# Kernel optimization log

Hardware: AMD Instinct MI355X
Metric: run time of the kernel (lower is better)

## Reference

```python
import jax, jax.numpy as jnp
import numpy as np

N = 256        # num_nodes
F = 256        # feature_dim
B = 32         # batch
DEG = 32       # out-degree per node -> E = N*DEG edges


def setup_inputs() -> dict:
    key = jax.random.key(0)
    k1, k2, k3, k4 = jax.random.split(key, 4)
    node_features = jax.random.normal(k1, (B, N, F), dtype=jnp.float32)
    # xavier_uniform for [N, N, F] tensor: fan_in = N*F, fan_out = N*F per torch default flattening
    limit = float(np.sqrt(6.0 / (N * F + N * F)))
    W = jax.random.uniform(k2, (N, N, F), dtype=jnp.float32, minval=-limit, maxval=limit)
    phase = jax.random.uniform(k3, (N, N), dtype=jnp.float32, minval=0.0, maxval=2.0 * np.pi)
    # topology: each node i has DEG outgoing connections (paths[i])
    src = jnp.repeat(jnp.arange(N, dtype=jnp.int64), DEG)              # [E]
    dst = jax.random.randint(k4, (N * DEG,), 0, N, dtype=jnp.int64)    # [E]
    return {"node_features": node_features, "W": W, "phase": phase, "src": src, "dst": dst}


def reference(node_features, W, phase, src, dst):
    # real(exp(i*phase)) == cos(phase); per-edge effective weight [E, F]
    eff_w = W[src, dst, :] * jnp.cos(phase[src, dst])[:, None]
    # gather source node features and scale: [B, E, F]
    signal = node_features[:, src, :] * eff_w[None, :, :]
    # scatter-add into destination nodes
    propagated = jnp.zeros_like(node_features).at[:, dst, :].add(signal)
    # normalization by out-degree of each node index (matches original indexing)
    n = node_features.shape[1]
    counts = jnp.zeros((n,), dtype=node_features.dtype).at[src].add(1.0)
    norm = jnp.maximum(counts, 1.0)
    return propagated / norm[None, :, None]
```

## Files before the change

kernel.cpp:

```cpp
#include <hip/hip_runtime.h>
#include <math.h>

#define NN 256
#define FF 256
#define BB 32
#define EE 8192
#define F4  (FF / 4)
#define NF4 (NN * F4)


#define CAP 64

__global__ __launch_bounds__(1024, 8) void fused_propagate_kernel(
    const float4* __restrict__ nf4,
    const float4* __restrict__ W4,
    const float*  __restrict__ phase,
    const int*    __restrict__ dst,
    float4*       __restrict__ out4)
{
    const int bid = blockIdx.x;
    const int d   = bid >> 1;
    const int h   = bid & 1;

    const int t    = threadIdx.x;
    const int lane = t & 63;
    const int wv   = t >> 6;

    __shared__ int          scnt[NN];
    __shared__ unsigned int s_pk[CAP / 4];
    __shared__ float        a_list[CAP];
    __shared__ int          wtot[4];
    __shared__ float4       aw4[CAP * 64];

    const int4* dstq = (const int4*)dst;
    const int4 v0 = dstq[t];
    const int4 v1 = dstq[t + 1024];
    int c0 = (v0.x == d) + (v0.y == d) + (v0.z == d) + (v0.w == d);
    int c1 = (v1.x == d) + (v1.y == d) + (v1.z == d) + (v1.w == d);
    #pragma unroll
    for (int off = 1; off < 8; off <<= 1) {
        c0 += __shfl_xor(c0, off, 64);
        c1 += __shfl_xor(c1, off, 64);
    }
    if ((t & 7) == 0) {
        scnt[t >> 3]         = c0;
        scnt[128 + (t >> 3)] = c1;
    }
    __syncthreads();

    int cnt = 0, ind = 0;
    if (t < NN) { cnt = scnt[t]; ind = (cnt > 0) ? 1 : 0; }

    const unsigned long long mask  = __ballot(ind);
    const int                below = __popcll(mask & ((1ULL << lane) - 1ULL));
    if (wv < 4 && lane == 0) wtot[wv] = __popcll(mask);
    __syncthreads();

    const int total = wtot[0] + wtot[1] + wtot[2] + wtot[3];
    int wbase = 0;
    #pragma unroll
    for (int w = 0; w < 4; w++) wbase += (w < wv) ? wtot[w] : 0;

    unsigned char* s8w = (unsigned char*)s_pk;
    if (ind) {
        const float a = (float)cnt * cosf(phase[t * NN + d]) * 0.03125f;
        const int pos = wbase + below;
        s8w[pos]    = (unsigned char)t;
        a_list[pos] = a;
    }
    const int n4 = (total + 3) & ~3;
    if (t < n4 - total) {
        s8w[total + t]    = 0;
        a_list[total + t] = 0.0f;
    }
    __syncthreads();

    const int drow = d * F4;
    const unsigned char* s8 = (const unsigned char*)s_pk;
    for (int slot = t; slot < (n4 << 6); slot += 1024) {
        const int   e = slot >> 6, f = slot & 63;
        const float a = a_list[e];
        float4 w = W4[(int)s8[e] * NF4 + drow + f];
        w.x *= a; w.y *= a; w.z *= a; w.w *= a;
        aw4[slot] = w;
    }
    __syncthreads();

    const int q = t & 63;
    const int b = h * 16 + (t >> 6);
    const float4* nfb = nf4 + b * NF4 + q;

    float4 acc = {0.f, 0.f, 0.f, 0.f};

    if (n4 > 0) {
        const unsigned int su = s_pk[0];
        float4 x0 = nfb[((su      ) & 255u) * 64];
        float4 x1 = nfb[((su >>  8) & 255u) * 64];
        float4 x2 = nfb[((su >> 16) & 255u) * 64];
        float4 x3 = nfb[((su >> 24)       ) * 64];

        for (int k = 4; k < n4; k += 4) {
            const unsigned int sn = s_pk[k >> 2];
            const float4 y0 = nfb[((sn      ) & 255u) * 64];
            const float4 y1 = nfb[((sn >>  8) & 255u) * 64];
            const float4 y2 = nfb[((sn >> 16) & 255u) * 64];
            const float4 y3 = nfb[((sn >> 24)       ) * 64];

            {
                const float4 a0 = aw4[(k - 4) * 64 + q];
                const float4 a1 = aw4[(k - 3) * 64 + q];
                const float4 a2 = aw4[(k - 2) * 64 + q];
                const float4 a3 = aw4[(k - 1) * 64 + q];
                acc.x = fmaf(x0.x, a0.x, acc.x); acc.y = fmaf(x0.y, a0.y, acc.y);
                acc.z = fmaf(x0.z, a0.z, acc.z); acc.w = fmaf(x0.w, a0.w, acc.w);
                acc.x = fmaf(x1.x, a1.x, acc.x); acc.y = fmaf(x1.y, a1.y, acc.y);
                acc.z = fmaf(x1.z, a1.z, acc.z); acc.w = fmaf(x1.w, a1.w, acc.w);
                acc.x = fmaf(x2.x, a2.x, acc.x); acc.y = fmaf(x2.y, a2.y, acc.y);
                acc.z = fmaf(x2.z, a2.z, acc.z); acc.w = fmaf(x2.w, a2.w, acc.w);
                acc.x = fmaf(x3.x, a3.x, acc.x); acc.y = fmaf(x3.y, a3.y, acc.y);
                acc.z = fmaf(x3.z, a3.z, acc.z); acc.w = fmaf(x3.w, a3.w, acc.w);
            }
            x0 = y0; x1 = y1; x2 = y2; x3 = y3;
        }

        {
            const float4 a0 = aw4[(n4 - 4) * 64 + q];
            const float4 a1 = aw4[(n4 - 3) * 64 + q];
            const float4 a2 = aw4[(n4 - 2) * 64 + q];
            const float4 a3 = aw4[(n4 - 1) * 64 + q];
            acc.x = fmaf(x0.x, a0.x, acc.x); acc.y = fmaf(x0.y, a0.y, acc.y);
            acc.z = fmaf(x0.z, a0.z, acc.z); acc.w = fmaf(x0.w, a0.w, acc.w);
            acc.x = fmaf(x1.x, a1.x, acc.x); acc.y = fmaf(x1.y, a1.y, acc.y);
            acc.z = fmaf(x1.z, a1.z, acc.z); acc.w = fmaf(x1.w, a1.w, acc.w);
            acc.x = fmaf(x2.x, a2.x, acc.x); acc.y = fmaf(x2.y, a2.y, acc.y);
            acc.z = fmaf(x2.z, a2.z, acc.z); acc.w = fmaf(x2.w, a2.w, acc.w);
            acc.x = fmaf(x3.x, a3.x, acc.x); acc.y = fmaf(x3.y, a3.y, acc.y);
            acc.z = fmaf(x3.z, a3.z, acc.z); acc.w = fmaf(x3.w, a3.w, acc.w);
        }
    }

    out4[b * NF4 + drow + q] = acc;
}

extern "C" void kernel_launch(void* const* d_in, const int* in_sizes, int n_in,
                              void* d_out, int out_size, void* d_ws, size_t ws_size,
                              hipStream_t stream) {
    const float* nf    = (const float*)d_in[0];
    const float* W     = (const float*)d_in[1];
    const float* phase = (const float*)d_in[2];
    const int*   dst   = (const int*)d_in[4];
    float*       out   = (float*)d_out;

    fused_propagate_kernel<<<512, 1024, 0, stream>>>(
        (const float4*)nf, (const float4*)W, phase, dst, (float4*)out);
}
```

Before: 117.9 us.

## Process all 32 batches per block and prefetch first features before weight staging

Each block now handles one destination node for all 32 batches (two accumulators per thread) instead of splitting batches across two blocks, halving the grid to 256 blocks. This avoids duplicating the dst histogram, phase/cos work and the W gather/scale into shared memory across two blocks. The first group of node-feature loads is also issued before the weight staging loop so their latency overlaps it. The cost is fewer blocks (256 for the whole GPU), more registers per thread and a lower launch-bounds occupancy hint.

New measurement: 114.6 us. -2.7%, faster.

```diff
diff --git a/kernel.cpp b/kernel.cpp
--- a/kernel.cpp
+++ b/kernel.cpp
@@ -11,17 +11,14 @@
 
 #define CAP 64
 
-__global__ __launch_bounds__(1024, 8) void fused_propagate_kernel(
+__global__ __launch_bounds__(1024, 4) void fused_propagate_kernel(
     const float4* __restrict__ nf4,
     const float4* __restrict__ W4,
     const float*  __restrict__ phase,
     const int*    __restrict__ dst,
     float4*       __restrict__ out4)
 {
-    const int bid = blockIdx.x;
-    const int d   = bid >> 1;
-    const int h   = bid & 1;
-
+    const int d    = blockIdx.x;
     const int t    = threadIdx.x;
     const int lane = t & 63;
     const int wv   = t >> 6;
@@ -75,6 +72,22 @@
     }
     __syncthreads();
 
+    const int q  = t & 63;
+    const int bg = t >> 6;
+    const float4* nfa = nf4 + bg * NF4 + q;
+    const float4* nfb = nf4 + (bg + 16) * NF4 + q;
+
+    float4 xa0, xa1, xa2, xa3, xb0, xb1, xb2, xb3;
+    {
+        const unsigned int su = s_pk[0];
+        const int sA = (int)(su & 255u), sB = (int)((su >> 8) & 255u);
+        const int sC = (int)((su >> 16) & 255u), sD = (int)(su >> 24);
+        xa0 = nfa[sA * 64]; xb0 = nfb[sA * 64];
+        xa1 = nfa[sB * 64]; xb1 = nfb[sB * 64];
+        xa2 = nfa[sC * 64]; xb2 = nfb[sC * 64];
+        xa3 = nfa[sD * 64]; xb3 = nfb[sD * 64];
+    }
+
     const int drow = d * F4;
     const unsigned char* s8 = (const unsigned char*)s_pk;
     for (int slot = t; slot < (n4 << 6); slot += 1024) {
@@ -86,41 +99,43 @@
     }
     __syncthreads();
 
-    const int q = t & 63;
-    const int b = h * 16 + (t >> 6);
-    const float4* nfb = nf4 + b * NF4 + q;
-
-    float4 acc = {0.f, 0.f, 0.f, 0.f};
+    float4 acc0 = {0.f, 0.f, 0.f, 0.f};
+    float4 acc1 = {0.f, 0.f, 0.f, 0.f};
 
     if (n4 > 0) {
-        const unsigned int su = s_pk[0];
-        float4 x0 = nfb[((su      ) & 255u) * 64];
-        float4 x1 = nfb[((su >>  8) & 255u) * 64];
-        float4 x2 = nfb[((su >> 16) & 255u) * 64];
-        float4 x3 = nfb[((su >> 24)       ) * 64];
-
         for (int k = 4; k < n4; k += 4) {
             const unsigned int sn = s_pk[k >> 2];
-            const float4 y0 = nfb[((sn      ) & 255u) * 64];
-            const float4 y1 = nfb[((sn >>  8) & 255u) * 64];
-            const float4 y2 = nfb[((sn >> 16) & 255u) * 64];
-            const float4 y3 = nfb[((sn >> 24)       ) * 64];
+            const int sE = (int)(sn & 255u), sF = (int)((sn >> 8) & 255u);
+            const int sG = (int)((sn >> 16) & 255u), sH = (int)(sn >> 24);
+            const float4 ya0 = nfa[sE * 64], yb0 = nfb[sE * 64];
+            const float4 ya1 = nfa[sF * 64], yb1 = nfb[sF * 64];
+            const float4 ya2 = nfa[sG * 64], yb2 = nfb[sG * 64];
+            const float4 ya3 = nfa[sH * 64], yb3 = nfb[sH * 64];
 
             {
                 const float4 a0 = aw4[(k - 4) * 64 + q];
                 const float4 a1 = aw4[(k - 3) * 64 + q];
                 const float4 a2 = aw4[(k - 2) * 64 + q];
                 const float4 a3 = aw4[(k - 1) * 64 + q];
-                acc.x = fmaf(x0.x, a0.x, acc.x); acc.y = fmaf(x0.y, a0.y, acc.y);
-                acc.z = fmaf(x0.z, a0.z, acc.z); acc.w = fmaf(x0.w, a0.w, acc.w);
-                acc.x = fmaf(x1.x, a1.x, acc.x); acc.y = fmaf(x1.y, a1.y, acc.y);
-                acc.z = fmaf(x1.z, a1.z, acc.z); acc.w = fmaf(x1.w, a1.w, acc.w);
-                acc.x = fmaf(x2.x, a2.x, acc.x); acc.y = fmaf(x2.y, a2.y, acc.y);
-                acc.z = fmaf(x2.z, a2.z, acc.z); acc.w = fmaf(x2.w, a2.w, acc.w);
-                acc.x = fmaf(x3.x, a3.x, acc.x); acc.y = fmaf(x3.y, a3.y, acc.y);
-                acc.z = fmaf(x3.z, a3.z, acc.z); acc.w = fmaf(x3.w, a3.w, acc.w);
+                acc0.x = fmaf(xa0.x, a0.x, acc0.x); acc0.y = fmaf(xa0.y, a0.y, acc0.y);
+                acc0.z = fmaf(xa0.z, a0.z, acc0.z); acc0.w = fmaf(xa0.w, a0.w, acc0.w);
+                acc1.x = fmaf(xb0.x, a0.x, acc1.x); acc1.y = fmaf(xb0.y, a0.y, acc1.y);
+                acc1.z = fmaf(xb0.z, a0.z, acc1.z); acc1.w = fmaf(xb0.w, a0.w, acc1.w);
+                acc0.x = fmaf(xa1.x, a1.x, acc0.x); acc0.y = fmaf(xa1.y, a1.y, acc0.y);
+                acc0.z = fmaf(xa1.z, a1.z, acc0.z); acc0.w = fmaf(xa1.w, a1.w, acc0.w);
+                acc1.x = fmaf(xb1.x, a1.x, acc1.x); acc1.y = fmaf(xb1.y, a1.y, acc1.y);
+                acc1.z = fmaf(xb1.z, a1.z, acc1.z); acc1.w = fmaf(xb1.w, a1.w, acc1.w);
+                acc0.x = fmaf(xa2.x, a2.x, acc0.x); acc0.y = fmaf(xa2.y, a2.y, acc0.y);
+                acc0.z = fmaf(xa2.z, a2.z, acc0.z); acc0.w = fmaf(xa2.w, a2.w, acc0.w);
+                acc1.x = fmaf(xb2.x, a2.x, acc1.x); acc1.y = fmaf(xb2.y, a2.y, acc1.y);
+                acc1.z = fmaf(xb2.z, a2.z, acc1.z); acc1.w = fmaf(xb2.w, a2.w, acc1.w);
+                acc0.x = fmaf(xa3.x, a3.x, acc0.x); acc0.y = fmaf(xa3.y, a3.y, acc0.y);
+                acc0.z = fmaf(xa3.z, a3.z, acc0.z); acc0.w = fmaf(xa3.w, a3.w, acc0.w);
+                acc1.x = fmaf(xb3.x, a3.x, acc1.x); acc1.y = fmaf(xb3.y, a3.y, acc1.y);
+                acc1.z = fmaf(xb3.z, a3.z, acc1.z); acc1.w = fmaf(xb3.w, a3.w, acc1.w);
             }
-            x0 = y0; x1 = y1; x2 = y2; x3 = y3;
+            xa0 = ya0; xa1 = ya1; xa2 = ya2; xa3 = ya3;
+            xb0 = yb0; xb1 = yb1; xb2 = yb2; xb3 = yb3;
         }
 
         {
@@ -128,18 +143,27 @@
             const float4 a1 = aw4[(n4 - 3) * 64 + q];
             const float4 a2 = aw4[(n4 - 2) * 64 + q];
             const float4 a3 = aw4[(n4 - 1) * 64 + q];
-            acc.x = fmaf(x0.x, a0.x, acc.x); acc.y = fmaf(x0.y, a0.y, acc.y);
-            acc.z = fmaf(x0.z, a0.z, acc.z); acc.w = fmaf(x0.w, a0.w, acc.w);
-            acc.x = fmaf(x1.x, a1.x, acc.x); acc.y = fmaf(x1.y, a1.y, acc.y);
-            acc.z = fmaf(x1.z, a1.z, acc.z); acc.w = fmaf(x1.w, a1.w, acc.w);
-            acc.x = fmaf(x2.x, a2.x, acc.x); acc.y = fmaf(x2.y, a2.y, acc.y);
-            acc.z = fmaf(x2.z, a2.z, acc.z); acc.w = fmaf(x2.w, a2.w, acc.w);
-            acc.x = fmaf(x3.x, a3.x, acc.x); acc.y = fmaf(x3.y, a3.y, acc.y);
-            acc.z = fmaf(x3.z, a3.z, acc.z); acc.w = fmaf(x3.w, a3.w, acc.w);
+            acc0.x = fmaf(xa0.x, a0.x, acc0.x); acc0.y = fmaf(xa0.y, a0.y, acc0.y);
+            acc0.z = fmaf(xa0.z, a0.z, acc0.z); acc0.w = fmaf(xa0.w, a0.w, acc0.w);
+            acc1.x = fmaf(xb0.x, a0.x, acc1.x); acc1.y = fmaf(xb0.y, a0.y, acc1.y);
+            acc1.z = fmaf(xb0.z, a0.z, acc1.z); acc1.w = fmaf(xb0.w, a0.w, acc1.w);
+            acc0.x = fmaf(xa1.x, a1.x, acc0.x); acc0.y = fmaf(xa1.y, a1.y, acc0.y);
+            acc0.z = fmaf(xa1.z, a1.z, acc0.z); acc0.w = fmaf(xa1.w, a1.w, acc0.w);
+            acc1.x = fmaf(xb1.x, a1.x, acc1.x); acc1.y = fmaf(xb1.y, a1.y, acc1.y);
+            acc1.z = fmaf(xb1.z, a1.z, acc1.z); acc1.w = fmaf(xb1.w, a1.w, acc1.w);
+            acc0.x = fmaf(xa2.x, a2.x, acc0.x); acc0.y = fmaf(xa2.y, a2.y, acc0.y);
+            acc0.z = fmaf(xa2.z, a2.z, acc0.z); acc0.w = fmaf(xa2.w, a2.w, acc0.w);
+            acc1.x = fmaf(xb2.x, a2.x, acc1.x); acc1.y = fmaf(xb2.y, a2.y, acc1.y);
+            acc1.z = fmaf(xb2.z, a2.z, acc1.z); acc1.w = fmaf(xb2.w, a2.w, acc1.w);
+            acc0.x = fmaf(xa3.x, a3.x, acc0.x); acc0.y = fmaf(xa3.y, a3.y, acc0.y);
+            acc0.z = fmaf(xa3.z, a3.z, acc0.z); acc0.w = fmaf(xa3.w, a3.w, acc0.w);
+            acc1.x = fmaf(xb3.x, a3.x, acc1.x); acc1.y = fmaf(xb3.y, a3.y, acc1.y);
+            acc1.z = fmaf(xb3.z, a3.z, acc1.z); acc1.w = fmaf(xb3.w, a3.w, acc1.w);
         }
     }
 
-    out4[b * NF4 + drow + q] = acc;
+    out4[bg * NF4 + drow + q]        = acc0;
+    out4[(bg + 16) * NF4 + drow + q] = acc1;
 }
 
 extern "C" void kernel_launch(void* const* d_in, const int* in_sizes, int n_in,
@@ -151,6 +175,6 @@
     const int*   dst   = (const int*)d_in[4];
     float*       out   = (float*)d_out;
 
-    fused_propagate_kernel<<<512, 1024, 0, stream>>>(
+    fused_propagate_kernel<<<NN, 1024, 0, stream>>>(
         (const float4*)nf, (const float4*)W, phase, dst, (float4*)out);
 }
```
